# Kernel tuning notes

Hardware: AMD Instinct MI355X
Metric: run time of the kernel (lower is better)

Reference implementation:

```python
import jax, jax.numpy as jnp
import numpy as np

B, S, HID = 4, 2048, 2048
NH, NKV = 8, 1
HD = HID // NH  # 256
G = NH // NKV   # queries per kv head
ROPE_THETA = 10000.0
NEG_INF = -1e9


def setup_inputs() -> dict:
    key = jax.random.key(0)
    ks = jax.random.split(key, 4)
    x = jax.random.normal(ks[0], (B, S, HID), jnp.float32)
    qkv_dim = (NH + 2 * NKV) * HD
    w_qkv = jax.random.normal(ks[1], (HID, qkv_dim), jnp.float32) * (HID ** -0.5)
    b_qkv = jnp.zeros((qkv_dim,), jnp.float32)
    w_o = jax.random.normal(ks[2], (NH * HD, HID), jnp.float32) * ((NH * HD) ** -0.5)
    b_o = jnp.zeros((HID,), jnp.float32)
    # rotary table: cos/sin of position*inv_freq, interleaved-pair convention
    inv_freq = 1.0 / (ROPE_THETA ** (jnp.arange(0, HD, 2, dtype=jnp.float32) / HD))
    ang = jnp.outer(jnp.arange(S, dtype=jnp.float32), inv_freq)  # [S, HD/2]
    freqs_cis = jnp.stack([jnp.cos(ang), jnp.sin(ang)], axis=-1)  # [S, HD/2, 2]
    causal = jnp.tril(jnp.ones((S, S), bool))
    mask = jnp.where(causal, 0.0, NEG_INF).astype(jnp.float32)[None, None]  # [1,1,S,S]
    return dict(x=x, w_qkv=w_qkv, b_qkv=b_qkv, w_o=w_o, b_o=b_o,
                freqs_cis=freqs_cis, mask=mask)


def _rope(t, cos, sin):
    # t: [B,S,H,D]; cos/sin: [1,S,1,D/2]; interleaved complex pairs
    tp = t.reshape(*t.shape[:-1], -1, 2)
    r, i = tp[..., 0], tp[..., 1]
    out = jnp.stack([r * cos - i * sin, r * sin + i * cos], axis=-1)
    return out.reshape(t.shape)


def reference(x, w_qkv, b_qkv, w_o, b_o, freqs_cis, mask):
    b, s, _ = x.shape
    qkv = x @ w_qkv + b_qkv
    q, k, v = jnp.split(qkv, [NH * HD, NH * HD + NKV * HD], axis=-1)
    q = q.reshape(b, s, NH, HD)
    k = k.reshape(b, s, NKV, HD)
    v = v.reshape(b, s, NKV, HD)
    cos = freqs_cis[..., 0][None, :, None, :]
    sin = freqs_cis[..., 1][None, :, None, :]
    q = _rope(q, cos, sin)
    k = _rope(k, cos, sin)
    # GQA: head h attends with kv group h // G (same layout as repeat_interleave)
    qh = q.transpose(0, 2, 1, 3).reshape(b, NKV, G, s, HD)  # [B,KV,G,S,D]
    kh = k.transpose(0, 2, 1, 3)                            # [B,KV,S,D]
    vh = v.transpose(0, 2, 1, 3)
    scores = jnp.einsum('bkgqd,bksd->bkgqs', qh, kh) * (HD ** -0.5)
    scores = scores + mask[:, :, None]  # broadcast over group dim
    attn = jax.nn.softmax(scores.astype(jnp.float32), axis=-1).astype(q.dtype)
    out = jnp.einsum('bkgqs,bksd->bkgqd', attn, vh)         # [B,KV,G,S,D]
    out = out.reshape(b, NH, s, HD).transpose(0, 2, 1, 3).reshape(b, s, NH * HD)
    return out @ w_o + b_o
```

## Files before the change

### kernel.cpp

```cpp
#include <hip/hip_runtime.h>
#include <hip/hip_bf16.h>

#define B_ 4
#define S_ 2048
#define HID_ 2048
#define NH_ 8
#define HD_ 256
#define QKVN 2560

typedef unsigned short u16;
typedef unsigned long long ull;
typedef __attribute__((ext_vector_type(4))) float f32x4;
typedef __attribute__((ext_vector_type(16))) float f32x16;
typedef __attribute__((ext_vector_type(8))) short bf16x8;

__device__ __forceinline__ float bf2f(u16 u) {
  union { unsigned int i; float f; } v; v.i = ((unsigned int)u) << 16; return v.f;
}
__device__ __forceinline__ u16 f2bf(float f) {
  union { unsigned int i; float f; } v; v.f = f;
  unsigned int r = v.i + 0x7fffu + ((v.i >> 16) & 1u);
  return (u16)(r >> 16);
}

// ... 61 lines not shown
  } while (0)

#define LOAD_A(buf, mib)                                                                          \
  _Pragma("unroll") for (int mi = 0; mi < 4; ++mi)                                                \
  _Pragma("unroll") for (int ks = 0; ks < 2; ++ks)                                                \
    af[mi][ks] = *(const bf16x8*)((buf) + (wr * 128 + ((mib) + mi) * 16 + l15) * 64 +             \
                                  (((ks * 4 + lg) ^ (l15 & 7)) << 3));

#define LOAD_B(buf, nib)                                                                          \
  _Pragma("unroll") for (int ni = 0; ni < 2; ++ni)                                                \
  _Pragma("unroll") for (int ks = 0; ks < 2; ++ks)                                                \
    bfr[(nib) + ni][ks] = *(const bf16x8*)((buf) + (wc * 64 + ((nib) + ni) * 16 + l15) * 64 +     \
                                           (((ks * 4 + lg) ^ (l15 & 7)) << 3));

#define MFMA16(accb, nib)                                                                         \
  _Pragma("unroll") for (int mi = 0; mi < 4; ++mi)                                                \
  _Pragma("unroll") for (int ni = 0; ni < 2; ++ni)                                                \
  _Pragma("unroll") for (int ks = 0; ks < 2; ++ks)                                                \
    acc[(accb) + mi][(nib) + ni] = __builtin_amdgcn_mfma_f32_16x16x32_bf16(                       \
        af[mi][ks], bfr[(nib) + ni][ks], acc[(accb) + mi][(nib) + ni], 0, 0, 0);

template <bool OUT_F32>
__global__ __launch_bounds__(512, 2) void gemm256(const u16* __restrict__ A, const u16* __restrict__ BT,
                                                  const float* __restrict__ bias, void* __restrict__ Cout,
                                                  int M, int N, int K) {
  __shared__ u16 Asm[2][16384];
  __shared__ u16 Bsm[2][16384];
  int nwg = gridDim.x;
  int bid = (int)blockIdx.x;
  bid = (bid & 7) * (nwg >> 3) + (bid >> 3);
  int ntn = N >> 8;
  int m0 = (bid / ntn) << 8, n0 = (bid % ntn) << 8;
  int tid = threadIdx.x, w = tid >> 6, lane = tid & 63;
  int wr = w >> 2, wc = w & 3;
  int l15 = lane & 15, lg = lane >> 4;
  int NT = K >> 6;
  u16* A0b = &Asm[0][0]; u16* A1b = &Asm[1][0];
  u16* B0b = &Bsm[0][0]; u16* B1b = &Bsm[1][0];
  f32x4 acc[8][4] = {};
  bf16x8 af[4][2], bfr[4][2];

  STG(A, m0, 0, 0, A0b); STG(A, m0, 1, 0, A0b);
  STG(BT, n0, 0, 0, B0b); STG(BT, n0, 1, 0, B0b);
  STG(A, m0, 0, 1, A1b); STG(BT, n0, 0, 1, B1b);
  WVM(0);
  BAR();

  for (int T = 0; T + 2 < NT; T += 2) {
    LOAD_A(A0b, 0); LOAD_B(B0b, 0);
    STG(A, m0, 1, T + 1, A1b);
    BAR(); PRIO1(); MFMA16(0, 0); PRIO0(); BAR();
    LOAD_B(B0b, 2);
    STG(BT, n0, 1, T + 1, B1b);
    BAR(); PRIO1(); MFMA16(0, 2); PRIO0(); BAR();
    LOAD_A(A0b, 4);
    STG(BT, n0, 0, T + 2, B0b);
    BAR(); PRIO1(); MFMA16(4, 0); PRIO0(); BAR();
    STG(A, m0, 0, T + 2, A0b);
    WVM(4);
    BAR(); PRIO1(); MFMA16(4, 2); PRIO0(); BAR();
    LOAD_A(A1b, 0); LOAD_B(B1b, 0);
    STG(A, m0, 1, T + 2, A0b);
    BAR(); PRIO1(); MFMA16(0, 0); PRIO0(); BAR();
    LOAD_B(B1b, 2);
    STG(BT, n0, 1, T + 2, B0b);
    BAR(); PRIO1(); MFMA16(0, 2); PRIO0(); BAR();
    LOAD_A(A1b, 4);
    STG(BT, n0, 0, T + 3, B1b);
    BAR(); PRIO1(); MFMA16(4, 0); PRIO0(); BAR();
    STG(A, m0, 0, T + 3, A1b);
    WVM(4);
    BAR(); PRIO1(); MFMA16(4, 2); PRIO0(); BAR();
  }
  {
    int T = NT - 2;
    LOAD_A(A0b, 0); LOAD_B(B0b, 0);
    STG(A, m0, 1, T + 1, A1b);
    BAR(); PRIO1(); MFMA16(0, 0); PRIO0(); BAR();
    LOAD_B(B0b, 2);
    STG(BT, n0, 1, T + 1, B1b);
    BAR(); PRIO1(); MFMA16(0, 2); PRIO0(); BAR();
    LOAD_A(A0b, 4);
    BAR(); PRIO1(); MFMA16(4, 0); PRIO0(); BAR();
    WVM(0);
    BAR(); PRIO1(); MFMA16(4, 2); PRIO0(); BAR();
    LOAD_A(A1b, 0); LOAD_B(B1b, 0);
    BAR(); PRIO1(); MFMA16(0, 0); PRIO0(); BAR();
    LOAD_B(B1b, 2);
    BAR(); PRIO1(); MFMA16(0, 2); PRIO0(); BAR();
    LOAD_A(A1b, 4);
    BAR(); PRIO1(); MFMA16(4, 0); PRIO0(); BAR();
    PRIO1(); MFMA16(4, 2); PRIO0();
  }
#pragma unroll
  for (int mi = 0; mi < 8; ++mi) {
    int mrow = m0 + wr * 128 + mi * 16 + lg * 4;
#pragma unroll
    for (int ni = 0; ni < 4; ++ni) {
      int col = n0 + wc * 64 + ni * 16 + l15;
      float bv = bias[col];
#pragma unroll
      for (int j = 0; j < 4; ++j) {
        float v = acc[mi][ni][j] + bv;
        if (OUT_F32)
          ((float*)Cout)[(size_t)(mrow + j) * N + col] = v;
        else
          ((u16*)Cout)[(size_t)(mrow + j) * N + col] = f2bf(v);
      }
    }
  }
}

__global__ void rope_scatter(const u16* __restrict__ qkv, const float* __restrict__ freqs,
                             u16* __restrict__ qo, u16* __restrict__ ko, u16* __restrict__ vo) {
  const int per_row = QKVN / 8;
  const int total = B_ * S_ * per_row;
  int i = blockIdx.x * blockDim.x + threadIdx.x;
  int stride = gridDim.x * blockDim.x;
  for (; i < total; i += stride) {
    int m = i / per_row;
    int n8 = (i - m * per_row) * 8;
    int b = m >> 11, s = m & 2047;
    uint4 raw = *(const uint4*)(qkv + (size_t)m * QKVN + n8);
    const u16* u = (const u16*)&raw;
    if (n8 < 2304) {
      int d = (n8 < 2048) ? (n8 & 255) : (n8 - 2048);
      float scl = (n8 < 2048) ? (0.0625f * 1.44269504f) : 1.0f;
      const float* fp = freqs + ((size_t)s * 128 + (d >> 1)) * 2;
      float4 f0 = *(const float4*)fp;
      float4 f1 = *(const float4*)(fp + 4);
      float fc[8] = {f0.x, f0.y, f0.z, f0.w, f1.x, f1.y, f1.z, f1.w};
      u16 o[8];
#pragma unroll
      for (int p = 0; p < 4; ++p) {
        float r = bf2f(u[2 * p]), im = bf2f(u[2 * p + 1]);
        float c = fc[2 * p], sn = fc[2 * p + 1];
        o[2 * p] = f2bf((r * c - im * sn) * scl);
        o[2 * p + 1] = f2bf((r * sn + im * c) * scl);
      }
      u16* dst;
      if (n8 < 2048) {
        dst = qo + (size_t)m * 2048 + n8;
      } else {
        dst = ko + (((size_t)m) << 8) + d;
      }
      *(uint4*)dst = *(const uint4*)o;
    } else {
      int d = n8 - 2304;
      *(uint4*)(vo + (((size_t)m) << 8) + d) = raw;
    }
  }
}

#define STAGE_K(bufofs, kt)                                                                       \
  do {                                                                                            \
    _Pragma("unroll") for (int _p = 0; _p < 4; ++_p) {                                            \
      int _idx = _p * 512 + tid;                                                                  \
      int _row = _idx >> 5, _c = _idx & 31;                                                       \
      const u16* _src = Kp + ((size_t)(b * S_ + (kt) * 64 + _row)) * HD_ +                        \
                        ((_c ^ (_row & 31)) * 8);                                                 \
      __builtin_amdgcn_global_load_lds(                                                           \
          (const __attribute__((address_space(1))) void*)_src,                                    \
          (__attribute__((address_space(3))) void*)(KsBase + (bufofs) + _idx * 8), 16, 0, 0);     \
    }                                                                                             \
  } while (0)

#define STAGE_V(bufofs, kt)                                                                       \
  do {                                                                                            \
    _Pragma("unroll") for (int _p = 0; _p < 4; ++_p) {                                            \
      int _idx = _p * 512 + tid;                                                                  \
      int _r = _idx >> 4, _gp = _idx & 15;                                                        \
      int _g = _gp ^ (_r & 15);                                                                   \
      int _d = _r * 2 + (_g >> 3), _c = _g & 7;                                                   \
      const u16* _src = VTp + ((size_t)(b * 256 + _d)) * S_ + (kt) * 64 + _c * 8;                 \
      __builtin_amdgcn_global_load_lds(                                                           \
          (const __attribute__((address_space(1))) void*)_src,                                    \
          (__attribute__((address_space(3))) void*)(VsBase + (bufofs) + _idx * 8), 16, 0, 0);     \
    }                                                                                             \
  } while (0)

#define FLASH_SEG_BODY()                                                                          \
  STAGE_K(0, kb);                                                                                 \
  STAGE_V(0, kb);                                                                                 \
  __syncthreads();                                                                                \
  int cur = 0;                                                                                    \
  for (int kt = kb; kt < ke; ++kt) {                                                              \
    if (kt + 1 < ke) {                                                                            \
      STAGE_K((cur ^ 1) * 16384, kt + 1);                                                         \
      STAGE_V((cur ^ 1) * 16384, kt + 1);                                                         \
    }                                                                                             \
    const char* Kb = (const char*)(KsBase + cur * 16384);                                         \
    const char* Vb = (const char*)(VsBase + cur * 16384);                                         \
    _Pragma("unroll") for (int tau = 0; tau < 2; ++tau) {                                         \
      int k0 = kt * 64 + tau * 32;                                                                \
      if (k0 > t * 32 + 31) break;                                                                \
      int row = tau * 32 + l31;                                                                   \
      f32x16 scv = {};                                                                            \
      __builtin_amdgcn_s_setprio(1);                                                              \
      _Pragma("unroll") for (int st = 0; st < 16; ++st) {                                         \
        bf16x8 kf = *(const bf16x8*)(Kb + row * 512 + (((st * 2 + lh) ^ l31) << 4));              \
        scv = __builtin_amdgcn_mfma_f32_32x32x16_bf16(kf, qf[st], scv, 0, 0, 0);                  \
      }                                                                                           \
      __builtin_amdgcn_s_setprio(0);                                                              \
      if (k0 + 31 > t * 32) {                                                                     \
        _Pragma("unroll") for (int jj = 0; jj < 16; ++jj) {                                       \
          int kg = k0 + (jj & 3) + 8 * (jj >> 2) + 4 * lh;                                        \
          if (kg > s_g) scv[jj] = -3.0e38f;                                                       \
        }                                                                                         \
      }                                                                                           \
      float tmax = -3.0e38f;                                                                      \
      _Pragma("unroll") for (int jj = 0; jj < 16; ++jj) tmax = fmaxf(tmax, scv[jj]);              \
      tmax = fmaxf(tmax, __shfl_xor(tmax, 32));                                                   \
      if (!__all(tmax - m_r <= 8.0f)) {                                                           \
        float mnew = fmaxf(m_r, tmax);                                                            \
        float sc = exp2f(m_r - mnew);                                                             \
        l_r *= sc;                                                                                \
        _Pragma("unroll") for (int dt = 0; dt < 8; ++dt) oacc[dt] *= sc;                          \
        m_r = mnew;                                                                               \
      }                                                                                           \
      float ts = 0.f;                                                                             \
      unsigned cpk[8];                                                                            \
      _Pragma("unroll") for (int mi = 0; mi < 8; ++mi) {                                          \
        float p0 = exp2f(scv[2 * mi] - m_r);                                                      \
        float p1 = exp2f(scv[2 * mi + 1] - m_r);                                                  \
        ts += p0 + p1;                                                                            \
        cpk[mi] = ((unsigned)f2bf(p1) << 16) | f2bf(p0);                                          \
      }                                                                                           \
      ts += __shfl_xor(ts, 32);                                                                   \
      l_r += ts;                                                                                  \
      asm volatile("v_permlane32_swap_b32 %0, %1" : "+v"(cpk[0]), "+v"(cpk[2]));                  \
      asm volatile("v_permlane32_swap_b32 %0, %1" : "+v"(cpk[1]), "+v"(cpk[3]));                  \
      asm volatile("v_permlane32_swap_b32 %0, %1" : "+v"(cpk[4]), "+v"(cpk[6]));                  \
      asm volatile("v_permlane32_swap_b32 %0, %1" : "+v"(cpk[5]), "+v"(cpk[7]));                  \
      union { unsigned u[4]; bf16x8 v; } pa, pb;                                                  \
      pa.u[0] = cpk[0]; pa.u[1] = cpk[1]; pa.u[2] = cpk[2]; pa.u[3] = cpk[3];                     \
      pb.u[0] = cpk[4]; pb.u[1] = cpk[5]; pb.u[2] = cpk[6]; pb.u[3] = cpk[7];                     \
      __builtin_amdgcn_s_setprio(1);                                                              \
      _Pragma("unroll") for (int dt = 0; dt < 8; ++dt) {                                          \
        int d = dt * 32 + l31;                                                                    \
        int rr = d >> 1;                                                                          \
        int gb = (d & 1) * 8 + tau * 4;                                                           \
        int rx = (rr & 15) << 4;                                                                  \
        bf16x8 va = *(const bf16x8*)(Vb + rr * 256 + (((gb + lh) << 4) ^ rx));                    \
        oacc[dt] = __builtin_amdgcn_mfma_f32_32x32x16_bf16(va, pa.v, oacc[dt], 0, 0, 0);          \
        bf16x8 vb2 = *(const bf16x8*)(Vb + rr * 256 + (((gb + 2 + lh) << 4) ^ rx));               \
        oacc[dt] = __builtin_amdgcn_mfma_f32_32x32x16_bf16(vb2, pb.v, oacc[dt], 0, 0, 0);         \
      }                                                                                           \
      __builtin_amdgcn_s_setprio(0);                                                              \
    }                                                                                             \
    __syncthreads();                                                                              \
    cur ^= 1;                                                                                     \
  }

__global__ __launch_bounds__(512, 2) void flash_attn(const u16* __restrict__ Qp, const u16* __restrict__ Kp,
                                                     const u16* __restrict__ VTp, u16* __restrict__ Op) {
  __shared__ u16 Ks[2][64 * 256];
  __shared__ u16 Vs[2][128 * 128];
  int bid = (int)blockIdx.x;
  int b = bid & 3, t = bid >> 2;
  int tid = threadIdx.x;
  int w = tid >> 6, l = tid & 63;
  int l31 = l & 31, lh = l >> 5;
  int q_local = w * 32 + l31;
  size_t qrow = (size_t)b * 16384 + (size_t)t * 256 + q_local;
  int s_g = t * 32 + (q_local >> 3);
  u16* KsBase = &Ks[0][0];
  u16* VsBase = &Vs[0][0];
  bf16x8 qf[16];
  const u16* qp = Qp + qrow * HD_ + lh * 8;
#pragma unroll
  for (int st = 0; st < 16; ++st) qf[st] = *(const bf16x8*)(qp + st * 16);
  f32x16 oacc[8] = {};
  float m_r = -3.0e38f, l_r = 0.f;
  int kb = 0, ke = t / 2 + 1;
  FLASH_SEG_BODY();
  float inv = 1.0f / l_r;
  u16* ob = Op + qrow * 256;
#pragma unroll
  for (int dt = 0; dt < 8; ++dt) {
#pragma unroll
    for (int jj = 0; jj < 4; ++jj) {
      int d0 = dt * 32 + jj * 8 + 4 * lh;
      u16 o4[4];
#pragma unroll
      for (int e = 0; e < 4; ++e) o4[e] = f2bf(oacc[dt][jj * 4 + e] * inv);
      *(ull*)(ob + d0) = *(const ull*)o4;
    }
  }
}

__global__ __launch_bounds__(512, 2) void flash_attn_split(const u16* __restrict__ Qp, const u16* __restrict__ Kp,
                                                           const u16* __restrict__ VTp, u16* __restrict__ P0,
                                                           float* __restrict__ ml0, float* __restrict__ ml1,
                                                           u16* __restrict__ Op) {
  __shared__ u16 Ks[2][64 * 256];
  __shared__ u16 Vs[2][128 * 128];
  int bid = (int)blockIdx.x;
  int b = (bid & 7) >> 1;
  int j = ((bid & 1) << 5) + (bid >> 3);
  int tid = threadIdx.x;
  int w = tid >> 6, l = tid & 63;
  int l31 = l & 31, lh = l >> 5;
  int q_local = w * 32 + l31;
  u16* KsBase = &Ks[0][0];
  u16* VsBase = &Vs[0][0];

  for (int seg = 0; seg < 2; ++seg) {
    int t = seg ? (63 - j) : j;
    int nkv = (t >> 1) + 1;
    int half = (nkv + 1) >> 1;
    int kb = seg ? half : 0;
    int ke = seg ? nkv : half;
    size_t qrow = (size_t)b * 16384 + (size_t)t * 256 + q_local;
    int s_g = t * 32 + (q_local >> 3);
    float* mlbuf = seg ? ml1 : ml0;
    if (kb >= ke) {
      if (lh == 0) { mlbuf[qrow * 2] = -3.0e38f; mlbuf[qrow * 2 + 1] = 0.f; }
      continue;
    }
    bf16x8 qf[16];
    const u16* qp = Qp + qrow * HD_ + lh * 8;
#pragma unroll
    for (int st = 0; st < 16; ++st) qf[st] = *(const bf16x8*)(qp + st * 16);
    f32x16 oacc[8] = {};
    float m_r = -3.0e38f, l_r = 0.f;
    FLASH_SEG_BODY();
    float inv = 1.0f / l_r;
    u16* ob = (seg ? Op : P0) + qrow * 256;
#pragma unroll
    for (int dt = 0; dt < 8; ++dt) {
#pragma unroll
      for (int jj = 0; jj < 4; ++jj) {
        int d0 = dt * 32 + jj * 8 + 4 * lh;
        u16 o4[4];
#pragma unroll
        for (int e = 0; e < 4; ++e) o4[e] = f2bf(oacc[dt][jj * 4 + e] * inv);
        *(ull*)(ob + d0) = *(const ull*)o4;
      }
    }
    if (lh == 0) { mlbuf[qrow * 2] = m_r; mlbuf[qrow * 2 + 1] = l_r; }
  }
}

__global__ __launch_bounds__(256) void combine_parts(const u16* __restrict__ P0, const float* __restrict__ ml0,
                                                     const float* __restrict__ ml1, u16* __restrict__ O) {
  int idx = blockIdx.x * 256 + threadIdx.x;
  int r = idx >> 5;
  int c = (idx & 31) * 8;
  float m0 = ml0[(size_t)r * 2], l0 = ml0[(size_t)r * 2 + 1];
  float m1 = ml1[(size_t)r * 2], l1 = ml1[(size_t)r * 2 + 1];
  float M = fmaxf(m0, m1);
  float w0 = l0 * exp2f(m0 - M), w1 = l1 * exp2f(m1 - M);
  float inv = 1.0f / (w0 + w1);
  w0 *= inv; w1 *= inv;
  uint4 a = *(const uint4*)(P0 + (size_t)r * 256 + c);
  uint4 bq = *(const uint4*)(O + (size_t)r * 256 + c);
  const u16* ua = (const u16*)&a;
  const u16* ub = (const u16*)&bq;
  u16 o[8];
#pragma unroll
  for (int e = 0; e < 8; ++e) o[e] = f2bf(w0 * bf2f(ua[e]) + w1 * bf2f(ub[e]));
  *(uint4*)(O + (size_t)r * 256 + c) = *(const uint4*)o;
}

extern "C" void kernel_launch(void* const* d_in, const int* in_sizes, int n_in,
                              void* d_out, int out_size, void* d_ws, size_t ws_size,
                              hipStream_t stream) {
  const float* x = (const float*)d_in[0];
  const float* w_qkv = (const float*)d_in[1];
  const float* b_qkv = (const float*)d_in[2];
  const float* w_o = (const float*)d_in[3];
  const float* b_o = (const float*)d_in[4];
  const float* freqs = (const float*)d_in[5];

  char* ws = (char*)d_ws;
  u16* xb    = (u16*)ws;
  u16* wqkvT = (u16*)(ws + 33554432);
  u16* woT   = (u16*)(ws + 44040192);
  u16* qkv   = (u16*)(ws + 52428800);
  u16* qall  = (u16*)(ws + 94371840);
  u16* kbuf  = (u16*)(ws + 127926272);
  u16* vbuf  = (u16*)(ws + 132120576);
  u16* part0 = (u16*)(ws + 136314880);
  float* ml0 = (float*)(ws + 169869312);
  float* ml1 = (float*)(ws + 170393600);
  u16* vT    = xb;
  u16* attout = qkv;

  bool split = (ws_size >= 170917888ULL);

  cast_f32_bf16<<<2048, 256, 0, stream>>>(x, xb, (B_ * S_ * HID_) / 8);
  transpose_cast<<<dim3(QKVN / 32, HID_ / 32), dim3(32, 8), 0, stream>>>(w_qkv, wqkvT, HID_, QKVN);
  transpose_cast<<<dim3(HID_ / 32, HID_ / 32), dim3(32, 8), 0, stream>>>(w_o, woT, HID_, HID_);
  gemm256<false><<<dim3(32 * 10), 512, 0, stream>>>(xb, wqkvT, b_qkv, qkv, B_ * S_, QKVN, HID_);
  rope_scatter<<<2048, 256, 0, stream>>>(qkv, freqs, qall, kbuf, vbuf);
  transpose_bf16<<<dim3(HD_ / 32, S_ / 32, B_), dim3(32, 8), 0, stream>>>(vbuf, vT, S_, HD_);
  if (split) {
    flash_attn_split<<<256, 512, 0, stream>>>(qall, kbuf, vT, part0, ml0, ml1, attout);
    combine_parts<<<8192, 256, 0, stream>>>(part0, ml0, ml1, attout);
  } else {
    flash_attn<<<256, 512, 0, stream>>>(qall, kbuf, vT, attout);
  }
  gemm256<true><<<dim3(32 * 8), 512, 0, stream>>>(attout, woT, b_o, d_out, B_ * S_, HID_, HID_);
}
```

Before: 398.0 us.

## Process two query tiles per wave in split flash attention to reuse K/V fragments

Each wave now handles 64 query rows (two 32-row tiles A and B) instead of 32, so every K and V fragment read from LDS feeds two MFMAs. The block shrinks from 512 to 256 threads with launch bounds (256,1), and the staging loops are adjusted to cover the same tile with fewer threads. The non-split fallback kernel is removed and the split path is always used. This halves LDS fragment reads per MFMA but doubles accumulator and Q registers per thread, lowering occupancy and risking spills.

```diff
diff --git a/kernel.cpp b/kernel.cpp
--- a/kernel.cpp
+++ b/kernel.cpp
@@ -237,10 +237,11 @@
   }
 }
 
-#define STAGE_K(bufofs, kt)                                                                       \
+
+#define STAGE_K2(bufofs, kt)                                                                      \
   do {                                                                                            \
-    _Pragma("unroll") for (int _p = 0; _p < 4; ++_p) {                                            \
-      int _idx = _p * 512 + tid;                                                                  \
+    _Pragma("unroll") for (int _p = 0; _p < 8; ++_p) {                                            \
+      int _idx = _p * 256 + tid;                                                                  \
       int _row = _idx >> 5, _c = _idx & 31;                                                       \
       const u16* _src = Kp + ((size_t)(b * S_ + (kt) * 64 + _row)) * HD_ +                        \
                         ((_c ^ (_row & 31)) * 8);                                                 \
@@ -250,10 +251,10 @@
     }                                                                                             \
   } while (0)
 
-#define STAGE_V(bufofs, kt)                                                                       \
+#define STAGE_V2(bufofs, kt)                                                                      \
   do {                                                                                            \
-    _Pragma("unroll") for (int _p = 0; _p < 4; ++_p) {                                            \
-      int _idx = _p * 512 + tid;                                                                  \
+    _Pragma("unroll") for (int _p = 0; _p < 8; ++_p) {                                            \
+      int _idx = _p * 256 + tid;                                                                  \
       int _r = _idx >> 4, _gp = _idx & 15;                                                        \
       int _g = _gp ^ (_r & 15);                                                                   \
       int _d = _r * 2 + (_g >> 3), _c = _g & 7;                                                   \
@@ -264,117 +265,7 @@
     }                                                                                             \
   } while (0)
 
-#define FLASH_SEG_BODY()                                                                          \
-  STAGE_K(0, kb);                                                                                 \
-  STAGE_V(0, kb);                                                                                 \
-  __syncthreads();                                                                                \
-  int cur = 0;                                                                                    \
-  for (int kt = kb; kt < ke; ++kt) {                                                              \
-    if (kt + 1 < ke) {                                                                            \
-      STAGE_K((cur ^ 1) * 16384, kt + 1);                                                         \
-      STAGE_V((cur ^ 1) * 16384, kt + 1);                                                         \
-    }                                                                                             \
-    const char* Kb = (const char*)(KsBase + cur * 16384);                                         \
-    const char* Vb = (const char*)(VsBase + cur * 16384);                                         \
-    _Pragma("unroll") for (int tau = 0; tau < 2; ++tau) {                                         \
-      int k0 = kt * 64 + tau * 32;                                                                \
-      if (k0 > t * 32 + 31) break;                                                                \
-      int row = tau * 32 + l31;                                                                   \
-      f32x16 scv = {};                                                                            \
-      __builtin_amdgcn_s_setprio(1);                                                              \
-      _Pragma("unroll") for (int st = 0; st < 16; ++st) {                                         \
-        bf16x8 kf = *(const bf16x8*)(Kb + row * 512 + (((st * 2 + lh) ^ l31) << 4));              \
-        scv = __builtin_amdgcn_mfma_f32_32x32x16_bf16(kf, qf[st], scv, 0, 0, 0);                  \
-      }                                                                                           \
-      __builtin_amdgcn_s_setprio(0);                                                              \
-      if (k0 + 31 > t * 32) {                                                                     \
-        _Pragma("unroll") for (int jj = 0; jj < 16; ++jj) {                                       \
-          int kg = k0 + (jj & 3) + 8 * (jj >> 2) + 4 * lh;                                        \
-          if (kg > s_g) scv[jj] = -3.0e38f;                                                       \
-        }                                                                                         \
-      }                                                                                           \
-      float tmax = -3.0e38f;                                                                      \
-      _Pragma("unroll") for (int jj = 0; jj < 16; ++jj) tmax = fmaxf(tmax, scv[jj]);              \
-      tmax = fmaxf(tmax, __shfl_xor(tmax, 32));                                                   \
-      if (!__all(tmax - m_r <= 8.0f)) {                                                           \
-        float mnew = fmaxf(m_r, tmax);                                                            \
-        float sc = exp2f(m_r - mnew);                                                             \
-        l_r *= sc;                                                                                \
-        _Pragma("unroll") for (int dt = 0; dt < 8; ++dt) oacc[dt] *= sc;                          \
-        m_r = mnew;                                                                               \
-      }                                                                                           \
-      float ts = 0.f;                                                                             \
-      unsigned cpk[8];                                                                            \
-      _Pragma("unroll") for (int mi = 0; mi < 8; ++mi) {                                          \
-        float p0 = exp2f(scv[2 * mi] - m_r);                                                      \
-        float p1 = exp2f(scv[2 * mi + 1] - m_r);                                                  \
-        ts += p0 + p1;                                                                            \
-        cpk[mi] = ((unsigned)f2bf(p1) << 16) | f2bf(p0);                                          \
-      }                                                                                           \
-      ts += __shfl_xor(ts, 32);                                                                   \
-      l_r += ts;                                                                                  \
-      asm volatile("v_permlane32_swap_b32 %0, %1" : "+v"(cpk[0]), "+v"(cpk[2]));                  \
-      asm volatile("v_permlane32_swap_b32 %0, %1" : "+v"(cpk[1]), "+v"(cpk[3]));                  \
-      asm volatile("v_permlane32_swap_b32 %0, %1" : "+v"(cpk[4]), "+v"(cpk[6]));                  \
-      asm volatile("v_permlane32_swap_b32 %0, %1" : "+v"(cpk[5]), "+v"(cpk[7]));                  \
-      union { unsigned u[4]; bf16x8 v; } pa, pb;                                                  \
-      pa.u[0] = cpk[0]; pa.u[1] = cpk[1]; pa.u[2] = cpk[2]; pa.u[3] = cpk[3];                     \
-      pb.u[0] = cpk[4]; pb.u[1] = cpk[5]; pb.u[2] = cpk[6]; pb.u[3] = cpk[7];                     \
-      __builtin_amdgcn_s_setprio(1);                                                              \
-      _Pragma("unroll") for (int dt = 0; dt < 8; ++dt) {                                          \
-        int d = dt * 32 + l31;                                                                    \
-        int rr = d >> 1;                                                                          \
-        int gb = (d & 1) * 8 + tau * 4;                                                           \
-        int rx = (rr & 15) << 4;                                                                  \
-        bf16x8 va = *(const bf16x8*)(Vb + rr * 256 + (((gb + lh) << 4) ^ rx));                    \
-        oacc[dt] = __builtin_amdgcn_mfma_f32_32x32x16_bf16(va, pa.v, oacc[dt], 0, 0, 0);          \
-        bf16x8 vb2 = *(const bf16x8*)(Vb + rr * 256 + (((gb + 2 + lh) << 4) ^ rx));               \
-        oacc[dt] = __builtin_amdgcn_mfma_f32_32x32x16_bf16(vb2, pb.v, oacc[dt], 0, 0, 0);         \
-      }                                                                                           \
-      __builtin_amdgcn_s_setprio(0);                                                              \
-    }                                                                                             \
-    __syncthreads();                                                                              \
-    cur ^= 1;                                                                                     \
-  }
-
-__global__ __launch_bounds__(512, 2) void flash_attn(const u16* __restrict__ Qp, const u16* __restrict__ Kp,
-                                                     const u16* __restrict__ VTp, u16* __restrict__ Op) {
-  __shared__ u16 Ks[2][64 * 256];
-  __shared__ u16 Vs[2][128 * 128];
-  int bid = (int)blockIdx.x;
-  int b = bid & 3, t = bid >> 2;
-  int tid = threadIdx.x;
-  int w = tid >> 6, l = tid & 63;
-  int l31 = l & 31, lh = l >> 5;
-  int q_local = w * 32 + l31;
-  size_t qrow = (size_t)b * 16384 + (size_t)t * 256 + q_local;
-  int s_g = t * 32 + (q_local >> 3);
-  u16* KsBase = &Ks[0][0];
-  u16* VsBase = &Vs[0][0];
-  bf16x8 qf[16];
-  const u16* qp = Qp + qrow * HD_ + lh * 8;
-#pragma unroll
-  for (int st = 0; st < 16; ++st) qf[st] = *(const bf16x8*)(qp + st * 16);
-  f32x16 oacc[8] = {};
-  float m_r = -3.0e38f, l_r = 0.f;
-  int kb = 0, ke = t / 2 + 1;
-  FLASH_SEG_BODY();
-  float inv = 1.0f / l_r;
-  u16* ob = Op + qrow * 256;
-#pragma unroll
-  for (int dt = 0; dt < 8; ++dt) {
-#pragma unroll
-    for (int jj = 0; jj < 4; ++jj) {
-      int d0 = dt * 32 + jj * 8 + 4 * lh;
-      u16 o4[4];
-#pragma unroll
-      for (int e = 0; e < 4; ++e) o4[e] = f2bf(oacc[dt][jj * 4 + e] * inv);
-      *(ull*)(ob + d0) = *(const ull*)o4;
-    }
-  }
-}
-
-__global__ __launch_bounds__(512, 2) void flash_attn_split(const u16* __restrict__ Qp, const u16* __restrict__ Kp,
+__global__ __launch_bounds__(256, 1) void flash_attn_split(const u16* __restrict__ Qp, const u16* __restrict__ Kp,
                                                            const u16* __restrict__ VTp, u16* __restrict__ P0,
                                                            float* __restrict__ ml0, float* __restrict__ ml1,
                                                            u16* __restrict__ Op) {
@@ -386,7 +277,6 @@
   int tid = threadIdx.x;
   int w = tid >> 6, l = tid & 63;
   int l31 = l & 31, lh = l >> 5;
-  int q_local = w * 32 + l31;
   u16* KsBase = &Ks[0][0];
   u16* VsBase = &Vs[0][0];
 
@@ -396,34 +286,155 @@
     int half = (nkv + 1) >> 1;
     int kb = seg ? half : 0;
     int ke = seg ? nkv : half;
-    size_t qrow = (size_t)b * 16384 + (size_t)t * 256 + q_local;
-    int s_g = t * 32 + (q_local >> 3);
+    int q0 = w * 64 + l31;
+    size_t qrowA = (size_t)b * 16384 + (size_t)t * 256 + q0;
+    size_t qrowB = qrowA + 32;
+    int sgA = t * 32 + (q0 >> 3);
+    int sgB = t * 32 + ((q0 + 32) >> 3);
     float* mlbuf = seg ? ml1 : ml0;
     if (kb >= ke) {
-      if (lh == 0) { mlbuf[qrow * 2] = -3.0e38f; mlbuf[qrow * 2 + 1] = 0.f; }
+      if (lh == 0) {
+        mlbuf[qrowA * 2] = -3.0e38f; mlbuf[qrowA * 2 + 1] = 0.f;
+        mlbuf[qrowB * 2] = -3.0e38f; mlbuf[qrowB * 2 + 1] = 0.f;
+      }
       continue;
     }
-    bf16x8 qf[16];
-    const u16* qp = Qp + qrow * HD_ + lh * 8;
-#pragma unroll
-    for (int st = 0; st < 16; ++st) qf[st] = *(const bf16x8*)(qp + st * 16);
-    f32x16 oacc[8] = {};
-    float m_r = -3.0e38f, l_r = 0.f;
-    FLASH_SEG_BODY();
-    float inv = 1.0f / l_r;
-    u16* ob = (seg ? Op : P0) + qrow * 256;
+    bf16x8 qfA[16], qfB[16];
+    {
+      const u16* qpA = Qp + qrowA * HD_ + lh * 8;
+      const u16* qpB = Qp + qrowB * HD_ + lh * 8;
+#pragma unroll
+      for (int st = 0; st < 16; ++st) {
+        qfA[st] = *(const bf16x8*)(qpA + st * 16);
+        qfB[st] = *(const bf16x8*)(qpB + st * 16);
+      }
+    }
+    f32x16 oaccA[8] = {}, oaccB[8] = {};
+    float mA = -3.0e38f, lA = 0.f, mB = -3.0e38f, lB = 0.f;
+
+    STAGE_K2(0, kb);
+    STAGE_V2(0, kb);
+    __syncthreads();
+    int cur = 0;
+    for (int kt = kb; kt < ke; ++kt) {
+      if (kt + 1 < ke) {
+        STAGE_K2((cur ^ 1) * 16384, kt + 1);
+        STAGE_V2((cur ^ 1) * 16384, kt + 1);
+      }
+      const char* Kb = (const char*)(KsBase + cur * 16384);
+      const char* Vb = (const char*)(VsBase + cur * 16384);
+#pragma unroll
+      for (int tau = 0; tau < 2; ++tau) {
+        int k0 = kt * 64 + tau * 32;
+        if (k0 > t * 32 + 31) break;
+        int row = tau * 32 + l31;
+        f32x16 svA = {}, svB = {};
+        __builtin_amdgcn_s_setprio(1);
+#pragma unroll
+        for (int st = 0; st < 16; ++st) {
+          bf16x8 kf = *(const bf16x8*)(Kb + row * 512 + (((st * 2 + lh) ^ l31) << 4));
+          svA = __builtin_amdgcn_mfma_f32_32x32x16_bf16(kf, qfA[st], svA, 0, 0, 0);
+          svB = __builtin_amdgcn_mfma_f32_32x32x16_bf16(kf, qfB[st], svB, 0, 0, 0);
+        }
+        __builtin_amdgcn_s_setprio(0);
+        if (k0 + 31 > t * 32) {
+#pragma unroll
+          for (int jj = 0; jj < 16; ++jj) {
+            int kg = k0 + (jj & 3) + 8 * (jj >> 2) + 4 * lh;
+            if (kg > sgA) svA[jj] = -3.0e38f;
+            if (kg > sgB) svB[jj] = -3.0e38f;
+          }
+        }
+        float tmA = -3.0e38f, tmB = -3.0e38f;
+#pragma unroll
+        for (int jj = 0; jj < 16; ++jj) { tmA = fmaxf(tmA, svA[jj]); tmB = fmaxf(tmB, svB[jj]); }
+        tmA = fmaxf(tmA, __shfl_xor(tmA, 32));
+        tmB = fmaxf(tmB, __shfl_xor(tmB, 32));
+        if (!__all(tmA - mA <= 8.0f)) {
+          float mnew = fmaxf(mA, tmA);
+          float sc = exp2f(mA - mnew);
+          lA *= sc;
+#pragma unroll
+          for (int dt = 0; dt < 8; ++dt) oaccA[dt] *= sc;
+          mA = mnew;
+        }
+        if (!__all(tmB - mB <= 8.0f)) {
+          float mnew = fmaxf(mB, tmB);
+          float sc = exp2f(mB - mnew);
+          lB *= sc;
+#pragma unroll
+          for (int dt = 0; dt < 8; ++dt) oaccB[dt] *= sc;
+          mB = mnew;
+        }
+        float tsA = 0.f, tsB = 0.f;
+        unsigned cpA[8], cpB[8];
+#pragma unroll
+        for (int mi = 0; mi < 8; ++mi) {
+          float a0 = exp2f(svA[2 * mi] - mA), a1 = exp2f(svA[2 * mi + 1] - mA);
+          float b0 = exp2f(svB[2 * mi] - mB), b1 = exp2f(svB[2 * mi + 1] - mB);
+          tsA += a0 + a1; tsB += b0 + b1;
+          cpA[mi] = ((unsigned)f2bf(a1) << 16) | f2bf(a0);
+          cpB[mi] = ((unsigned)f2bf(b1) << 16) | f2bf(b0);
+        }
+        tsA += __shfl_xor(tsA, 32);
+        tsB += __shfl_xor(tsB, 32);
+        lA += tsA;
+        lB += tsB;
+        asm volatile("v_permlane32_swap_b32 %0, %1" : "+v"(cpA[0]), "+v"(cpA[2]));
+        asm volatile("v_permlane32_swap_b32 %0, %1" : "+v"(cpA[1]), "+v"(cpA[3]));
+        asm volatile("v_permlane32_swap_b32 %0, %1" : "+v"(cpA[4]), "+v"(cpA[6]));
+        asm volatile("v_permlane32_swap_b32 %0, %1" : "+v"(cpA[5]), "+v"(cpA[7]));
+        asm volatile("v_permlane32_swap_b32 %0, %1" : "+v"(cpB[0]), "+v"(cpB[2]));
+        asm volatile("v_permlane32_swap_b32 %0, %1" : "+v"(cpB[1]), "+v"(cpB[3]));
+        asm volatile("v_permlane32_swap_b32 %0, %1" : "+v"(cpB[4]), "+v"(cpB[6]));
+        asm volatile("v_permlane32_swap_b32 %0, %1" : "+v"(cpB[5]), "+v"(cpB[7]));
+        union { unsigned u[4]; bf16x8 v; } paA, pbA, paB, pbB;
+        paA.u[0] = cpA[0]; paA.u[1] = cpA[1]; paA.u[2] = cpA[2]; paA.u[3] = cpA[3];
+        pbA.u[0] = cpA[4]; pbA.u[1] = cpA[5]; pbA.u[2] = cpA[6]; pbA.u[3] = cpA[7];
+        paB.u[0] = cpB[0]; paB.u[1] = cpB[1]; paB.u[2] = cpB[2]; paB.u[3] = cpB[3];
+        pbB.u[0] = cpB[4]; pbB.u[1] = cpB[5]; pbB.u[2] = cpB[6]; pbB.u[3] = cpB[7];
+        __builtin_amdgcn_s_setprio(1);
+#pragma unroll
+        for (int dt = 0; dt < 8; ++dt) {
+          int d = dt * 32 + l31;
+          int rr = d >> 1;
+          int gb = (d & 1) * 8 + tau * 4;
+          int rx = (rr & 15) << 4;
+          bf16x8 va = *(const bf16x8*)(Vb + rr * 256 + (((gb + lh) << 4) ^ rx));
+          oaccA[dt] = __builtin_amdgcn_mfma_f32_32x32x16_bf16(va, paA.v, oaccA[dt], 0, 0, 0);
+          oaccB[dt] = __builtin_amdgcn_mfma_f32_32x32x16_bf16(va, paB.v, oaccB[dt], 0, 0, 0);
+          bf16x8 vb2 = *(const bf16x8*)(Vb + rr * 256 + (((gb + 2 + lh) << 4) ^ rx));
+          oaccA[dt] = __builtin_amdgcn_mfma_f32_32x32x16_bf16(vb2, pbA.v, oaccA[dt], 0, 0, 0);
+          oaccB[dt] = __builtin_amdgcn_mfma_f32_32x32x16_bf16(vb2, pbB.v, oaccB[dt], 0, 0, 0);
+        }
+        __builtin_amdgcn_s_setprio(0);
+      }
+      __syncthreads();
+      cur ^= 1;
+    }
+
+    float invA = 1.0f / lA, invB = 1.0f / lB;
+    u16* obA = (seg ? Op : P0) + qrowA * 256;
+    u16* obB = (seg ? Op : P0) + qrowB * 256;
 #pragma unroll
     for (int dt = 0; dt < 8; ++dt) {
 #pragma unroll
       for (int jj = 0; jj < 4; ++jj) {
         int d0 = dt * 32 + jj * 8 + 4 * lh;
-        u16 o4[4];
-#pragma unroll
-        for (int e = 0; e < 4; ++e) o4[e] = f2bf(oacc[dt][jj * 4 + e] * inv);
-        *(ull*)(ob + d0) = *(const ull*)o4;
-      }
-    }
-    if (lh == 0) { mlbuf[qrow * 2] = m_r; mlbuf[qrow * 2 + 1] = l_r; }
+        u16 oA[4], oB[4];
+#pragma unroll
+        for (int e = 0; e < 4; ++e) {
+          oA[e] = f2bf(oaccA[dt][jj * 4 + e] * invA);
+          oB[e] = f2bf(oaccB[dt][jj * 4 + e] * invB);
+        }
+        *(ull*)(obA + d0) = *(const ull*)oA;
+        *(ull*)(obB + d0) = *(const ull*)oB;
+      }
+    }
+    if (lh == 0) {
+      mlbuf[qrowA * 2] = mA; mlbuf[qrowA * 2 + 1] = lA;
+      mlbuf[qrowB * 2] = mB; mlbuf[qrowB * 2 + 1] = lB;
+    }
   }
 }
 
@@ -472,19 +483,13 @@
   u16* vT    = xb;
   u16* attout = qkv;
 
-  bool split = (ws_size >= 170917888ULL);
-
   cast_f32_bf16<<<2048, 256, 0, stream>>>(x, xb, (B_ * S_ * HID_) / 8);
   transpose_cast<<<dim3(QKVN / 32, HID_ / 32), dim3(32, 8), 0, stream>>>(w_qkv, wqkvT, HID_, QKVN);
   transpose_cast<<<dim3(HID_ / 32, HID_ / 32), dim3(32, 8), 0, stream>>>(w_o, woT, HID_, HID_);
   gemm256<false><<<dim3(32 * 10), 512, 0, stream>>>(xb, wqkvT, b_qkv, qkv, B_ * S_, QKVN, HID_);
   rope_scatter<<<2048, 256, 0, stream>>>(qkv, freqs, qall, kbuf, vbuf);
   transpose_bf16<<<dim3(HD_ / 32, S_ / 32, B_), dim3(32, 8), 0, stream>>>(vbuf, vT, S_, HD_);
-  if (split) {
-    flash_attn_split<<<256, 512, 0, stream>>>(qall, kbuf, vT, part0, ml0, ml1, attout);
-    combine_parts<<<8192, 256, 0, stream>>>(part0, ml0, ml1, attout);
-  } else {
-    flash_attn<<<256, 512, 0, stream>>>(qall, kbuf, vT, attout);
-  }
+  flash_attn_split<<<256, 256, 0, stream>>>(qall, kbuf, vT, part0, ml0, ml1, attout);
+  combine_parts<<<8192, 256, 0, stream>>>(part0, ml0, ml1, attout);
   gemm256<true><<<dim3(32 * 8), 512, 0, stream>>>(attout, woT, b_o, d_out, B_ * S_, HID_, HID_);
 }
```

Result: slower. 991.6 us (+149.1%).

## Split attention KV range four ways with single-buffered LDS and 4-way combine

Applied to the files above, without the earlier changes.

Adds a flash_attn_split4 kernel that splits each query tile's causal KV range into four parts across 1024 blocks, writing partial outputs and (m,l) stats to four buffers, then merges them in a new combine_parts4 kernel. The new kernel uses single-buffered K/V in shared memory rather than double buffering, which lowers LDS use so more blocks can be resident, but it no longer overlaps loads with compute. The aim is better load balance and occupancy for the causal attention. The cost is extra partial-buffer traffic and a heavier combine step. The old two-way split becomes the fallback when the workspace is too small, and the unsplit kernel is removed.

```diff
diff --git a/kernel.cpp b/kernel.cpp
--- a/kernel.cpp
+++ b/kernel.cpp
@@ -264,115 +264,62 @@
     }                                                                                             \
   } while (0)
 
-#define FLASH_SEG_BODY()                                                                          \
-  STAGE_K(0, kb);                                                                                 \
-  STAGE_V(0, kb);                                                                                 \
-  __syncthreads();                                                                                \
-  int cur = 0;                                                                                    \
-  for (int kt = kb; kt < ke; ++kt) {                                                              \
-    if (kt + 1 < ke) {                                                                            \
-      STAGE_K((cur ^ 1) * 16384, kt + 1);                                                         \
-      STAGE_V((cur ^ 1) * 16384, kt + 1);                                                         \
-    }                                                                                             \
-    const char* Kb = (const char*)(KsBase + cur * 16384);                                         \
-    const char* Vb = (const char*)(VsBase + cur * 16384);                                         \
-    _Pragma("unroll") for (int tau = 0; tau < 2; ++tau) {                                         \
-      int k0 = kt * 64 + tau * 32;                                                                \
-      if (k0 > t * 32 + 31) break;                                                                \
-      int row = tau * 32 + l31;                                                                   \
-      f32x16 scv = {};                                                                            \
-      __builtin_amdgcn_s_setprio(1);                                                              \
-      _Pragma("unroll") for (int st = 0; st < 16; ++st) {                                         \
-        bf16x8 kf = *(const bf16x8*)(Kb + row * 512 + (((st * 2 + lh) ^ l31) << 4));              \
-        scv = __builtin_amdgcn_mfma_f32_32x32x16_bf16(kf, qf[st], scv, 0, 0, 0);                  \
+#define FLASH_TAU_BODY(Kbp, Vbp)                                                                  \
+  do {                                                                                            \
+    int row = tau * 32 + l31;                                                                     \
+    f32x16 scv = {};                                                                              \
+    __builtin_amdgcn_s_setprio(1);                                                                \
+    _Pragma("unroll") for (int st = 0; st < 16; ++st) {                                           \
+      bf16x8 kf = *(const bf16x8*)((Kbp) + row * 512 + (((st * 2 + lh) ^ l31) << 4));             \
+      scv = __builtin_amdgcn_mfma_f32_32x32x16_bf16(kf, qf[st], scv, 0, 0, 0);                    \
+    }                                                                                             \
+    __builtin_amdgcn_s_setprio(0);                                                                \
+    if (k0 + 31 > t * 32) {                                                                       \
+      _Pragma("unroll") for (int jj = 0; jj < 16; ++jj) {                                         \
+        int kg = k0 + (jj & 3) + 8 * (jj >> 2) + 4 * lh;                                          \
+        if (kg > s_g) scv[jj] = -3.0e38f;                                                         \
       }                                                                                           \
-      __builtin_amdgcn_s_setprio(0);                                                              \
-      if (k0 + 31 > t * 32) {                                                                     \
-        _Pragma("unroll") for (int jj = 0; jj < 16; ++jj) {                                       \
-          int kg = k0 + (jj & 3) + 8 * (jj >> 2) + 4 * lh;                                        \
-          if (kg > s_g) scv[jj] = -3.0e38f;                                                       \
-        }                                                                                         \
-      }                                                                                           \
-      float tmax = -3.0e38f;                                                                      \
-      _Pragma("unroll") for (int jj = 0; jj < 16; ++jj) tmax = fmaxf(tmax, scv[jj]);              \
-      tmax = fmaxf(tmax, __shfl_xor(tmax, 32));                                                   \
-      if (!__all(tmax - m_r <= 8.0f)) {                                                           \
-        float mnew = fmaxf(m_r, tmax);                                                            \
-        float sc = exp2f(m_r - mnew);                                                             \
-        l_r *= sc;                                                                                \
-        _Pragma("unroll") for (int dt = 0; dt < 8; ++dt) oacc[dt] *= sc;                          \
-        m_r = mnew;                                                                               \
-      }                                                                                           \
-      float ts = 0.f;                                                                             \
-      unsigned cpk[8];                                                                            \
-      _Pragma("unroll") for (int mi = 0; mi < 8; ++mi) {                                          \
-        float p0 = exp2f(scv[2 * mi] - m_r);                                                      \
-        float p1 = exp2f(scv[2 * mi + 1] - m_r);                                                  \
-        ts += p0 + p1;                                                                            \
-        cpk[mi] = ((unsigned)f2bf(p1) << 16) | f2bf(p0);                                          \
-      }                                                                                           \
-      ts += __shfl_xor(ts, 32);                                                                   \
-      l_r += ts;                                                                                  \
-      asm volatile("v_permlane32_swap_b32 %0, %1" : "+v"(cpk[0]), "+v"(cpk[2]));                  \
-      asm volatile("v_permlane32_swap_b32 %0, %1" : "+v"(cpk[1]), "+v"(cpk[3]));                  \
-      asm volatile("v_permlane32_swap_b32 %0, %1" : "+v"(cpk[4]), "+v"(cpk[6]));                  \
-      asm volatile("v_permlane32_swap_b32 %0, %1" : "+v"(cpk[5]), "+v"(cpk[7]));                  \
-      union { unsigned u[4]; bf16x8 v; } pa, pb;                                                  \
-      pa.u[0] = cpk[0]; pa.u[1] = cpk[1]; pa.u[2] = cpk[2]; pa.u[3] = cpk[3];                     \
-      pb.u[0] = cpk[4]; pb.u[1] = cpk[5]; pb.u[2] = cpk[6]; pb.u[3] = cpk[7];                     \
-      __builtin_amdgcn_s_setprio(1);                                                              \
-      _Pragma("unroll") for (int dt = 0; dt < 8; ++dt) {                                          \
-        int d = dt * 32 + l31;                                                                    \
-        int rr = d >> 1;                                                                          \
-        int gb = (d & 1) * 8 + tau * 4;                                                           \
-        int rx = (rr & 15) << 4;                                                                  \
-        bf16x8 va = *(const bf16x8*)(Vb + rr * 256 + (((gb + lh) << 4) ^ rx));                    \
-        oacc[dt] = __builtin_amdgcn_mfma_f32_32x32x16_bf16(va, pa.v, oacc[dt], 0, 0, 0);          \
-        bf16x8 vb2 = *(const bf16x8*)(Vb + rr * 256 + (((gb + 2 + lh) << 4) ^ rx));               \
-        oacc[dt] = __builtin_amdgcn_mfma_f32_32x32x16_bf16(vb2, pb.v, oacc[dt], 0, 0, 0);         \
-      }                                                                                           \
-      __builtin_amdgcn_s_setprio(0);                                                              \
-    }                                                                                             \
-    __syncthreads();                                                                              \
-    cur ^= 1;                                                                                     \
-  }
-
-__global__ __launch_bounds__(512, 2) void flash_attn(const u16* __restrict__ Qp, const u16* __restrict__ Kp,
-                                                     const u16* __restrict__ VTp, u16* __restrict__ Op) {
-  __shared__ u16 Ks[2][64 * 256];
-  __shared__ u16 Vs[2][128 * 128];
-  int bid = (int)blockIdx.x;
-  int b = bid & 3, t = bid >> 2;
-  int tid = threadIdx.x;
-  int w = tid >> 6, l = tid & 63;
-  int l31 = l & 31, lh = l >> 5;
-  int q_local = w * 32 + l31;
-  size_t qrow = (size_t)b * 16384 + (size_t)t * 256 + q_local;
-  int s_g = t * 32 + (q_local >> 3);
-  u16* KsBase = &Ks[0][0];
-  u16* VsBase = &Vs[0][0];
-  bf16x8 qf[16];
-  const u16* qp = Qp + qrow * HD_ + lh * 8;
-#pragma unroll
-  for (int st = 0; st < 16; ++st) qf[st] = *(const bf16x8*)(qp + st * 16);
-  f32x16 oacc[8] = {};
-  float m_r = -3.0e38f, l_r = 0.f;
-  int kb = 0, ke = t / 2 + 1;
-  FLASH_SEG_BODY();
-  float inv = 1.0f / l_r;
-  u16* ob = Op + qrow * 256;
-#pragma unroll
-  for (int dt = 0; dt < 8; ++dt) {
-#pragma unroll
-    for (int jj = 0; jj < 4; ++jj) {
-      int d0 = dt * 32 + jj * 8 + 4 * lh;
-      u16 o4[4];
-#pragma unroll
-      for (int e = 0; e < 4; ++e) o4[e] = f2bf(oacc[dt][jj * 4 + e] * inv);
-      *(ull*)(ob + d0) = *(const ull*)o4;
-    }
-  }
-}
+    }                                                                                             \
+    float tmax = -3.0e38f;                                                                        \
+    _Pragma("unroll") for (int jj = 0; jj < 16; ++jj) tmax = fmaxf(tmax, scv[jj]);                \
+    tmax = fmaxf(tmax, __shfl_xor(tmax, 32));                                                     \
+    if (!__all(tmax - m_r <= 8.0f)) {                                                             \
+      float mnew = fmaxf(m_r, tmax);                                                              \
+      float sc = exp2f(m_r - mnew);                                                               \
+      l_r *= sc;                                                                                  \
+      _Pragma("unroll") for (int dt = 0; dt < 8; ++dt) oacc[dt] *= sc;                            \
+      m_r = mnew;                                                                                 \
+    }                                                                                             \
+    float ts = 0.f;                                                                               \
+    unsigned cpk[8];                                                                              \
+    _Pragma("unroll") for (int mi = 0; mi < 8; ++mi) {                                            \
+      float p0 = exp2f(scv[2 * mi] - m_r);                                                        \
+      float p1 = exp2f(scv[2 * mi + 1] - m_r);                                                    \
+      ts += p0 + p1;                                                                              \
+      cpk[mi] = ((unsigned)f2bf(p1) << 16) | f2bf(p0);                                            \
+    }                                                                                             \
+    ts += __shfl_xor(ts, 32);                                                                     \
+    l_r += ts;                                                                                    \
+    asm volatile("v_permlane32_swap_b32 %0, %1" : "+v"(cpk[0]), "+v"(cpk[2]));                    \
+    asm volatile("v_permlane32_swap_b32 %0, %1" : "+v"(cpk[1]), "+v"(cpk[3]));                    \
+    asm volatile("v_permlane32_swap_b32 %0, %1" : "+v"(cpk[4]), "+v"(cpk[6]));                    \
+    asm volatile("v_permlane32_swap_b32 %0, %1" : "+v"(cpk[5]), "+v"(cpk[7]));                    \
+    union { unsigned u[4]; bf16x8 v; } pa, pb;                                                    \
+    pa.u[0] = cpk[0]; pa.u[1] = cpk[1]; pa.u[2] = cpk[2]; pa.u[3] = cpk[3];                       \
+    pb.u[0] = cpk[4]; pb.u[1] = cpk[5]; pb.u[2] = cpk[6]; pb.u[3] = cpk[7];                       \
+    __builtin_amdgcn_s_setprio(1);                                                                \
+    _Pragma("unroll") for (int dt = 0; dt < 8; ++dt) {                                            \
+      int d = dt * 32 + l31;                                                                      \
+      int rr = d >> 1;                                                                            \
+      int gb = (d & 1) * 8 + tau * 4;                                                             \
+      int rx = (rr & 15) << 4;                                                                    \
+      bf16x8 va = *(const bf16x8*)((Vbp) + rr * 256 + (((gb + lh) << 4) ^ rx));                   \
+      oacc[dt] = __builtin_amdgcn_mfma_f32_32x32x16_bf16(va, pa.v, oacc[dt], 0, 0, 0);            \
+      bf16x8 vb2 = *(const bf16x8*)((Vbp) + rr * 256 + (((gb + 2 + lh) << 4) ^ rx));              \
+      oacc[dt] = __builtin_amdgcn_mfma_f32_32x32x16_bf16(vb2, pb.v, oacc[dt], 0, 0, 0);           \
+    }                                                                                             \
+    __builtin_amdgcn_s_setprio(0);                                                                \
+  } while (0)
 
 __global__ __launch_bounds__(512, 2) void flash_attn_split(const u16* __restrict__ Qp, const u16* __restrict__ Kp,
                                                            const u16* __restrict__ VTp, u16* __restrict__ P0,
@@ -409,7 +356,26 @@
     for (int st = 0; st < 16; ++st) qf[st] = *(const bf16x8*)(qp + st * 16);
     f32x16 oacc[8] = {};
     float m_r = -3.0e38f, l_r = 0.f;
-    FLASH_SEG_BODY();
+    STAGE_K(0, kb);
+    STAGE_V(0, kb);
+    __syncthreads();
+    int cur = 0;
+    for (int kt = kb; kt < ke; ++kt) {
+      if (kt + 1 < ke) {
+        STAGE_K((cur ^ 1) * 16384, kt + 1);
+        STAGE_V((cur ^ 1) * 16384, kt + 1);
+      }
+      const char* Kb = (const char*)(KsBase + cur * 16384);
+      const char* Vb = (const char*)(VsBase + cur * 16384);
+#pragma unroll
+      for (int tau = 0; tau < 2; ++tau) {
+        int k0 = kt * 64 + tau * 32;
+        if (k0 > t * 32 + 31) break;
+        FLASH_TAU_BODY(Kb, Vb);
+      }
+      __syncthreads();
+      cur ^= 1;
+    }
     float inv = 1.0f / l_r;
     u16* ob = (seg ? Op : P0) + qrow * 256;
 #pragma unroll
@@ -448,6 +414,138 @@
   *(uint4*)(O + (size_t)r * 256 + c) = *(const uint4*)o;
 }
 
+#define STAGE_K1(kt)                                                                              \
+  do {                                                                                            \
+    _Pragma("unroll") for (int _p = 0; _p < 4; ++_p) {                                            \
+      int _idx = _p * 512 + tid;                                                                  \
+      int _row = _idx >> 5, _c = _idx & 31;                                                       \
+      const u16* _src = Kp + ((size_t)(b * S_ + (kt) * 64 + _row)) * HD_ +                        \
+                        ((_c ^ (_row & 31)) * 8);                                                 \
+      __builtin_amdgcn_global_load_lds(                                                           \
+          (const __attribute__((address_space(1))) void*)_src,                                    \
+          (__attribute__((address_space(3))) void*)(KsBase + _idx * 8), 16, 0, 0);                \
+    }                                                                                             \
+  } while (0)
+
+#define STAGE_V1(kt)                                                                              \
+  do {                                                                                            \
+    _Pragma("unroll") for (int _p = 0; _p < 4; ++_p) {                                            \
+      int _idx = _p * 512 + tid;                                                                  \
+      int _r = _idx >> 4, _gp = _idx & 15;                                                        \
+      int _g = _gp ^ (_r & 15);                                                                   \
+      int _d = _r * 2 + (_g >> 3), _c = _g & 7;                                                   \
+      const u16* _src = VTp + ((size_t)(b * 256 + _d)) * S_ + (kt) * 64 + _c * 8;                 \
+      __builtin_amdgcn_global_load_lds(                                                           \
+          (const __attribute__((address_space(1))) void*)_src,                                    \
+          (__attribute__((address_space(3))) void*)(VsBase + _idx * 8), 16, 0, 0);                \
+    }                                                                                             \
+  } while (0)
+
+__global__ __launch_bounds__(512, 2) void flash_attn_split4(const u16* __restrict__ Qp, const u16* __restrict__ Kp,
+                                                            const u16* __restrict__ VTp,
+                                                            u16* __restrict__ P0, u16* __restrict__ P1,
+                                                            u16* __restrict__ P2, u16* __restrict__ Op,
+                                                            float* __restrict__ ml0, float* __restrict__ ml1,
+                                                            float* __restrict__ ml2, float* __restrict__ ml3) {
+  __shared__ u16 Ks[64 * 256];
+  __shared__ u16 Vs[128 * 128];
+  int bid = (int)blockIdx.x;
+  int b = (bid & 7) >> 1;
+  int rest = ((bid & 1) << 7) | (bid >> 3);
+  int t = rest & 63;
+  int p = rest >> 6;
+  int tid = threadIdx.x;
+  int w = tid >> 6, l = tid & 63;
+  int l31 = l & 31, lh = l >> 5;
+  int q_local = w * 32 + l31;
+  u16* KsBase = &Ks[0];
+  u16* VsBase = &Vs[0];
+
+  int nkv = (t >> 1) + 1;
+  int kb = (nkv * p) >> 2;
+  int ke = (nkv * (p + 1)) >> 2;
+  size_t qrow = (size_t)b * 16384 + (size_t)t * 256 + q_local;
+  int s_g = t * 32 + (q_local >> 3);
+  u16* Obuf = (p == 0) ? P0 : (p == 1) ? P1 : (p == 2) ? P2 : Op;
+  float* mlbuf = (p == 0) ? ml0 : (p == 1) ? ml1 : (p == 2) ? ml2 : ml3;
+
+  if (kb >= ke) {
+    if (lh == 0) { mlbuf[qrow * 2] = -3.0e38f; mlbuf[qrow * 2 + 1] = 0.f; }
+    return;
+  }
+
+  bf16x8 qf[16];
+  const u16* qp = Qp + qrow * HD_ + lh * 8;
+#pragma unroll
+  for (int st = 0; st < 16; ++st) qf[st] = *(const bf16x8*)(qp + st * 16);
+  f32x16 oacc[8] = {};
+  float m_r = -3.0e38f, l_r = 0.f;
+
+  STAGE_K1(kb);
+  STAGE_V1(kb);
+  __syncthreads();
+  for (int kt = kb; kt < ke; ++kt) {
+#pragma unroll
+    for (int tau = 0; tau < 2; ++tau) {
+      int k0 = kt * 64 + tau * 32;
+      if (k0 > t * 32 + 31) break;
+      FLASH_TAU_BODY((const char*)KsBase, (const char*)VsBase);
+    }
+    __syncthreads();
+    if (kt + 1 < ke) {
+      STAGE_K1(kt + 1);
+      STAGE_V1(kt + 1);
+      __syncthreads();
+    }
+  }
+
+  float inv = 1.0f / l_r;
+  u16* ob = Obuf + qrow * 256;
+#pragma unroll
+  for (int dt = 0; dt < 8; ++dt) {
+#pragma unroll
+    for (int jj = 0; jj < 4; ++jj) {
+      int d0 = dt * 32 + jj * 8 + 4 * lh;
+      u16 o4[4];
+#pragma unroll
+      for (int e = 0; e < 4; ++e) o4[e] = f2bf(oacc[dt][jj * 4 + e] * inv);
+      *(ull*)(ob + d0) = *(const ull*)o4;
+    }
+  }
+  if (lh == 0) { mlbuf[qrow * 2] = m_r; mlbuf[qrow * 2 + 1] = l_r; }
+}
+
+__global__ __launch_bounds__(256) void combine_parts4(const u16* __restrict__ P0, const u16* __restrict__ P1,
+                                                      const u16* __restrict__ P2, const float* __restrict__ ml0,
+                                                      const float* __restrict__ ml1, const float* __restrict__ ml2,
+                                                      const float* __restrict__ ml3, u16* __restrict__ O) {
+  int idx = blockIdx.x * 256 + threadIdx.x;
+  int r = idx >> 5;
+  int c = (idx & 31) * 8;
+  float m0 = ml0[(size_t)r * 2], l0 = ml0[(size_t)r * 2 + 1];
+  float m1 = ml1[(size_t)r * 2], l1 = ml1[(size_t)r * 2 + 1];
+  float m2 = ml2[(size_t)r * 2], l2 = ml2[(size_t)r * 2 + 1];
+  float m3 = ml3[(size_t)r * 2], l3 = ml3[(size_t)r * 2 + 1];
+  float M = fmaxf(fmaxf(m0, m1), fmaxf(m2, m3));
+  float w0 = l0 * exp2f(m0 - M), w1 = l1 * exp2f(m1 - M);
+  float w2 = l2 * exp2f(m2 - M), w3 = l3 * exp2f(m3 - M);
+  float inv = 1.0f / (w0 + w1 + w2 + w3);
+  w0 *= inv; w1 *= inv; w2 *= inv; w3 *= inv;
+  uint4 a0 = *(const uint4*)(P0 + (size_t)r * 256 + c);
+  uint4 a1 = *(const uint4*)(P1 + (size_t)r * 256 + c);
+  uint4 a2 = *(const uint4*)(P2 + (size_t)r * 256 + c);
+  uint4 a3 = *(const uint4*)(O + (size_t)r * 256 + c);
+  const u16* u0 = (const u16*)&a0;
+  const u16* u1 = (const u16*)&a1;
+  const u16* u2 = (const u16*)&a2;
+  const u16* u3 = (const u16*)&a3;
+  u16 o[8];
+#pragma unroll
+  for (int e = 0; e < 8; ++e)
+    o[e] = f2bf(w0 * bf2f(u0[e]) + w1 * bf2f(u1[e]) + w2 * bf2f(u2[e]) + w3 * bf2f(u3[e]));
+  *(uint4*)(O + (size_t)r * 256 + c) = *(const uint4*)o;
+}
+
 extern "C" void kernel_launch(void* const* d_in, const int* in_sizes, int n_in,
                               void* d_out, int out_size, void* d_ws, size_t ws_size,
                               hipStream_t stream) {
@@ -469,10 +567,14 @@
   u16* part0 = (u16*)(ws + 136314880);
   float* ml0 = (float*)(ws + 169869312);
   float* ml1 = (float*)(ws + 170393600);
+  u16* part1 = (u16*)(ws + 170917888);
+  u16* part2 = (u16*)(ws + 204472320);
+  float* ml2 = (float*)(ws + 33554432);
+  float* ml3 = (float*)(ws + 33554432 + 524288);
   u16* vT    = xb;
   u16* attout = qkv;
 
-  bool split = (ws_size >= 170917888ULL);
+  bool split4 = (ws_size >= 238026752ULL);
 
   cast_f32_bf16<<<2048, 256, 0, stream>>>(x, xb, (B_ * S_ * HID_) / 8);
   transpose_cast<<<dim3(QKVN / 32, HID_ / 32), dim3(32, 8), 0, stream>>>(w_qkv, wqkvT, HID_, QKVN);
@@ -480,11 +582,13 @@
   gemm256<false><<<dim3(32 * 10), 512, 0, stream>>>(xb, wqkvT, b_qkv, qkv, B_ * S_, QKVN, HID_);
   rope_scatter<<<2048, 256, 0, stream>>>(qkv, freqs, qall, kbuf, vbuf);
   transpose_bf16<<<dim3(HD_ / 32, S_ / 32, B_), dim3(32, 8), 0, stream>>>(vbuf, vT, S_, HD_);
-  if (split) {
+  if (split4) {
+    flash_attn_split4<<<1024, 512, 0, stream>>>(qall, kbuf, vT, part0, part1, part2, attout,
+                                                ml0, ml1, ml2, ml3);
+    combine_parts4<<<8192, 256, 0, stream>>>(part0, part1, part2, ml0, ml1, ml2, ml3, attout);
+  } else {
     flash_attn_split<<<256, 512, 0, stream>>>(qall, kbuf, vT, part0, ml0, ml1, attout);
     combine_parts<<<8192, 256, 0, stream>>>(part0, ml0, ml1, attout);
-  } else {
-    flash_attn<<<256, 512, 0, stream>>>(qall, kbuf, vT, attout);
   }
   gemm256<true><<<dim3(32 * 8), 512, 0, stream>>>(attout, woT, b_o, d_out, B_ * S_, HID_, HID_);
 }
```

New measurement: 464.7 us. +16.8%, slower.
